# Kernel tuning notes

Hardware: AMD Instinct MI355X
Metric: run time of the kernel (lower is better)

## Reference

```python
import jax, jax.numpy as jnp
import numpy as np

EPS = 1e-8


def setup_inputs() -> dict:
    key = jax.random.key(0)
    ks = jax.random.split(key, 8)
    B, N, D = 8, 1024, 256
    x = jax.random.normal(ks[0], (B, N, D), dtype=jnp.float32)
    y = jax.random.normal(ks[1], (B, N, D), dtype=jnp.float32)
    coords = jax.random.normal(ks[2], (N, N, 6), dtype=jnp.float32)
    # xavier-ish init for U, kaiming-ish for S1/S2
    U = jax.random.normal(ks[3], (D, D), dtype=jnp.float32) * (1.0 / np.sqrt(D))
    S1 = jax.random.normal(ks[4], (D, 1), dtype=jnp.float32)
    S2 = jax.random.normal(ks[5], (D, 1), dtype=jnp.float32)
    gating = jnp.asarray(1.0, dtype=jnp.float32)
    h_temp = jnp.asarray(0.1, dtype=jnp.float32)
    p_temp = jnp.asarray(1.0, dtype=jnp.float32)
    # trunc_normal_(a=0, b=1): std-normal truncated to [0, 1]
    pos_emb = jax.random.truncated_normal(ks[6], 0.0, 1.0, (N, 6, 1)).astype(jnp.float32)
    return {"x": x, "y": y, "coords": coords, "U": U, "S1": S1, "S2": S2,
            "gating": gating, "h_temp": h_temp, "p_temp": p_temp, "pos_emb": pos_emb}


def _spectral(x, U, S):
    # x @ U.T @ diag(|S|) @ U  ==  ((x @ U.T) * |S|) @ U
    s = jnp.abs(S[:, 0])
    return ((x @ U.T) * s) @ U


def reference(x, y, coords, U, S1, S2, gating, h_temp, p_temp, pos_emb):
    B, N, D = x.shape
    scale = D ** (-0.5)
    xs = jnp.stack([_spectral(x, U, S1), _spectral(x, U, S2)], axis=1)  # [B,2,N,D]
    # patch attention scores: [B,2,N,N]
    patch_score = jax.nn.softmax(jnp.einsum('bknd,bmd->bknm', xs, y) * scale, axis=-1)
    # positional scores, shared across batch and the 2 spectral branches: [N,N]
    pos_logits = -jnp.abs(p_temp) * jnp.einsum('nmc,ncq->nm', coords, pos_emb)
    pos_score = jax.nn.softmax(pos_logits, axis=-1)
    g = jax.nn.sigmoid(gating)
    attn = (1.0 - g) * patch_score + g * pos_score[None, None]  # [B,2,N,N]
    # entropy over key axis -> [B,N,2]
    entropy = jnp.sum(-attn * jnp.log(attn + EPS), axis=-1).transpose(0, 2, 1)
    hmap = 2.0 - 2.0 * jax.nn.sigmoid(h_temp * entropy)  # [B,N,2]
    fgbg = hmap[..., 0] >= hmap[..., 1]
    route = jax.lax.stop_gradient(
        jnp.stack([fgbg, ~fgbg], axis=-1).astype(hmap.dtype))  # [B,N,2]
    heat_map = jnp.sum(hmap * route, axis=-1, keepdims=True)  # [B,N,1]
    attn_sel = jnp.sum(attn * route.transpose(0, 2, 1)[..., None], axis=1)  # [B,N,N]
    out = attn_sel @ y  # [B,N,D]
    return (out, heat_map)
```

## Files before the change

kernel.cpp:

```cpp
#include <hip/hip_runtime.h>
#include <hip/hip_bf16.h>
#include <stdint.h>


#define NB 8
#define NN_ 1024
#define ND 256

typedef __bf16 bf16x8 __attribute__((ext_vector_type(8)));
typedef __bf16 bf16x4 __attribute__((ext_vector_type(4)));
typedef float f32x4 __attribute__((ext_vector_type(4)));

__device__ inline void gl_lds(const __bf16* g, __bf16* l) {
    auto gp = (const __attribute__((address_space(1))) uint32_t*)(uintptr_t)g;
    auto lp = (__attribute__((address_space(3))) uint32_t*)(uintptr_t)l;
    __builtin_amdgcn_global_load_lds(gp, lp, 16, 0, 0);
}

__device__ inline float wred_sum(float v) {
#pragma unroll
    for (int o = 32; o; o >>= 1) v += __shfl_xor(v, o, 64);
    return v;
}
__device__ inline float wred_max(float v) {
#pragma unroll
    for (int o = 32; o; o >>= 1) v = fmaxf(v, __shfl_xor(v, o, 64));
    return v;
}

__global__ __launch_bounds__(256) void prep_kernel(
    const float* __restrict__ coords, const float* __restrict__ pos_emb,
    const float* __restrict__ p_temp, const float* __restrict__ x,
    const float* __restrict__ y, const float* __restrict__ U,
    const float* __restrict__ S1, const float* __restrict__ S2,
    float* __restrict__ posS, __bf16* __restrict__ Xh, __bf16* __restrict__ Xl,
    __bf16* __restrict__ yt, __bf16* __restrict__ Yh, __bf16* __restrict__ Yl,
    __bf16* __restrict__ Mh, __bf16* __restrict__ Ml) {
    __shared__ char sm[18432];
    const int bid = blockIdx.x;
    const int tid = threadIdx.x;

    if (bid < 256) {
        float* Us  = (float*)sm;
        float* s1s = Us + 16 * 256;
        float* s2s = s1s + 256;
        const int n = bid, j = tid;
        s1s[tid] = fabsf(S1[tid]);
        s2s[tid] = fabsf(S2[tid]);
        float a1 = 0.f, a2 = 0.f;
        for (int c0 = 0; c0 < ND; c0 += 16) {
            __syncthreads();
#pragma unroll
            for (int k = 0; k < 4; ++k) {
                const int idx = k * 256 + tid;
                ((float4*)Us)[idx] =
                    ((const float4*)(U + (long)c0 * ND))[idx];
            }
            __syncthreads();
#pragma unroll
            for (int cc = 0; cc < 16; ++cc) {
                const float un = Us[cc * 256 + n];
                const float uj = Us[cc * 256 + j];
                a1 = fmaf(s1s[c0 + cc] * un, uj, a1);
                a2 = fmaf(s2s[c0 + cc] * un, uj, a2);
            }
        }
        const __bf16 h1 = (__bf16)a1, h2 = (__bf16)a2;
        Mh[n * ND + j] = h1;           Ml[n * ND + j] = (__bf16)(a1 - (float)h1);
        Mh[65536 + n * ND + j] = h2;   Ml[65536 + n * ND + j] = (__bf16)(a2 - (float)h2);
    } else if (bid < 1280) {
        float* red = (float*)sm;
        const int n = bid - 256;
        const float pt = -fabsf(p_temp[0]);
        float pe[6];
#pragma unroll
        for (int c = 0; c < 6; ++c) pe[c] = pos_emb[n * 6 + c];
        const float* cr = coords + (long)n * NN_ * 6;
        float l[4];
#pragma unroll
        for (int j = 0; j < 4; ++j) {
            const int m = j * 256 + tid;
            const float2* cp = (const float2*)(cr + (long)m * 6);
            float2 c0 = cp[0], c1 = cp[1], c2 = cp[2];
            l[j] = pt * (c0.x * pe[0] + c0.y * pe[1] + c1.x * pe[2] +
                         c1.y * pe[3] + c2.x * pe[4] + c2.y * pe[5]);
        }
        float mx = fmaxf(fmaxf(l[0], l[1]), fmaxf(l[2], l[3]));
        mx = wred_max(mx);
        __syncthreads();
        if ((tid & 63) == 0) red[tid >> 6] = mx;
        __syncthreads();
        mx = fmaxf(fmaxf(red[0], red[1]), fmaxf(red[2], red[3]));
        float e[4], s = 0.f;
#pragma unroll
        for (int j = 0; j < 4; ++j) { e[j] = __expf(l[j] - mx); s += e[j]; }
        s = wred_sum(s);
        __syncthreads();
        if ((tid & 63) == 0) red[4 + (tid >> 6)] = s;
        __syncthreads();
        s = red[4] + red[5] + red[6] + red[7];
        const float inv = 1.f / s;
#pragma unroll
        for (int j = 0; j < 4; ++j)
            posS[(long)n * NN_ + j * 256 + tid] = e[j] * inv;
    } else if (bid < 1792) {
        const int n4 = NB * NN_ * ND / 4;
        int i = (bid - 1280) * 256 + tid;
        for (; i < n4; i += 512 * 256) {
            float4 v = ((const float4*)x)[i];
            bf16x4 h, l;
            h[0] = (__bf16)v.x; l[0] = (__bf16)(v.x - (float)h[0]);
            h[1] = (__bf16)v.y; l[1] = (__bf16)(v.y - (float)h[1]);
            h[2] = (__bf16)v.z; l[2] = (__bf16)(v.z - (float)h[2]);
            h[3] = (__bf16)v.w; l[3] = (__bf16)(v.w - (float)h[3]);
            ((bf16x4*)Xh)[i] = h;
            ((bf16x4*)Xl)[i] = l;
        }
    } else {
        __bf16 (*t)[72] = (__bf16(*)[72])sm;
        const int rem = bid - 1792;
        const int b = rem >> 6;
        const int m0 = (rem & 15) * 64, d0 = ((rem >> 4) & 3) * 64;
        const int c = tid & 15;
        const int r = tid >> 4;
#pragma unroll
        for (int p = 0; p < 4; ++p) {
            const int row = r + p * 16;
            const long gi = ((long)b * NN_ + m0 + row) * ND + d0 + c * 4;
            float4 v = *(const float4*)(y + gi);
            bf16x4 h, l;
            h[0] = (__bf16)v.x; l[0] = (__bf16)(v.x - (float)h[0]);
            h[1] = (__bf16)v.y; l[1] = (__bf16)(v.y - (float)h[1]);
            h[2] = (__bf16)v.z; l[2] = (__bf16)(v.z - (float)h[2]);
            h[3] = (__bf16)v.w; l[3] = (__bf16)(v.w - (float)h[3]);
            *(bf16x4*)(Yh + gi) = h;
            *(bf16x4*)(Yl + gi) = l;
            t[c * 4 + 0][row] = h[0]; t[c * 4 + 1][row] = h[1];
            t[c * 4 + 2][row] = h[2]; t[c * 4 + 3][row] = h[3];
        }
        __syncthreads();
#pragma unroll
        for (int p = 0; p < 4; ++p) {
            const int d = r + p * 16;
            bf16x4 o;
            o[0] = t[d][c * 4 + 0]; o[1] = t[d][c * 4 + 1];
            o[2] = t[d][c * 4 + 2]; o[3] = t[d][c * 4 + 3];
            *(bf16x4*)(yt + ((long)b * ND + d0 + d) * NN_ + m0 + c * 4) = o;
        }
    }
}

__global__ __launch_bounds__(256) void mgemm_xs(
    const __bf16* __restrict__ Ah, const __bf16* __restrict__ Al,
    const __bf16* __restrict__ Bh, const __bf16* __restrict__ Bl,
    __bf16* __restrict__ Ch, __bf16* __restrict__ Cl,
    int M, int N, int K, long sB1, long sC) {
    constexpr int BM = 64, BK = 32, BN = 64;
    __shared__ __bf16 As[2][2 * BM * BK];
    __shared__ __bf16 Bs[2][2 * BN * BK];

    const int z = blockIdx.z;
    Bh += (long)z * sB1; Bl += (long)z * sB1;

    const int tid = threadIdx.x;
    const int bm = blockIdx.y * BM, bn = blockIdx.x * BN;
    const int wave = tid >> 6, lane = tid & 63;
    const int wm = wave >> 1, wn = wave & 1;
    const int quad = lane >> 4, l16 = lane & 15;
    const int srow = lane >> 2, slot = lane & 3;

    f32x4 acc[2][2];
#pragma unroll
    for (int i = 0; i < 2; ++i)
#pragma unroll
        for (int j = 0; j < 2; ++j) acc[i][j] = (f32x4){0.f, 0.f, 0.f, 0.f};

    auto stage = [&](int sel, int k0) {
        const int r0 = wave * 16;
        const int row = r0 + srow;
        const int chunk = slot ^ ((row >> 1) & 3);
        const long ga = (long)(bm + row) * K + k0 + chunk * 8;
        gl_lds(Ah + ga, &As[sel][r0 * 32]);
        gl_lds(Al + ga, &As[sel][BM * BK + r0 * 32]);
        const long gb = (long)(bn + row) * K + k0 + chunk * 8;
        gl_lds(Bh + gb, &Bs[sel][r0 * 32]);
        gl_lds(Bl + gb, &Bs[sel][BN * BK + r0 * 32]);
    };

    stage(0, 0);
    __syncthreads();
    int cur = 0;
    for (int k0 = 0; k0 < K; k0 += BK) {
        if (k0 + BK < K) stage(cur ^ 1, k0 + BK);

        bf16x8 a_h[2], a_l[2], b_h[2], b_l[2];
#pragma unroll
        for (int mi = 0; mi < 2; ++mi) {
            const int row = wm * 32 + mi * 16 + l16;
            const int off = row * 32 + ((quad ^ ((row >> 1) & 3)) * 8);
            a_h[mi] = *(const bf16x8*)&As[cur][off];
            a_l[mi] = *(const bf16x8*)&As[cur][BM * BK + off];
        }
#pragma unroll
        for (int ni = 0; ni < 2; ++ni) {
            const int row = wn * 32 + ni * 16 + l16;
            const int off = row * 32 + ((quad ^ ((row >> 1) & 3)) * 8);
            b_h[ni] = *(const bf16x8*)&Bs[cur][off];
            b_l[ni] = *(const bf16x8*)&Bs[cur][BN * BK + off];
        }
#pragma unroll
        for (int mi = 0; mi < 2; ++mi)
#pragma unroll
            for (int ni = 0; ni < 2; ++ni) {
                acc[mi][ni] = __builtin_amdgcn_mfma_f32_16x16x32_bf16(
                    a_h[mi], b_h[ni], acc[mi][ni], 0, 0, 0);
                acc[mi][ni] = __builtin_amdgcn_mfma_f32_16x16x32_bf16(
                    a_h[mi], b_l[ni], acc[mi][ni], 0, 0, 0);
                acc[mi][ni] = __builtin_amdgcn_mfma_f32_16x16x32_bf16(
                    a_l[mi], b_h[ni], acc[mi][ni], 0, 0, 0);
            }

        __syncthreads();
        cur ^= 1;
    }

    Ch += (long)z * sC; Cl += (long)z * sC;
#pragma unroll
    for (int mi = 0; mi < 2; ++mi) {
        const int row0 = bm + wm * 32 + mi * 16 + quad * 4;
#pragma unroll
        for (int ni = 0; ni < 2; ++ni) {
            const int col = bn + wn * 32 + ni * 16 + l16;
#pragma unroll
            for (int r = 0; r < 4; ++r) {
                const float v = acc[mi][ni][r];
                const long idx = (long)(row0 + r) * N + col;
                const __bf16 h = (__bf16)v;
                Ch[idx] = h;
                Cl[idx] = (__bf16)(v - (float)h);
            }
        }
    }
}

__global__ __launch_bounds__(256) void mgemm_sc(
    const __bf16* __restrict__ Ah, const __bf16* __restrict__ Al,
    const __bf16* __restrict__ Bh, const __bf16* __restrict__ Bl,
    float* __restrict__ C, int N, int K,
    long sA1, long sA2, long sB1, long sC, float alpha) {
    constexpr int BM = 128, BK = 32, BN = 128;
    __shared__ __bf16 As[2 * BM * BK];
    __shared__ __bf16 Bs[2 * BN * BK];

    const int bid = blockIdx.x;
    const int xcd = bid & 7;
    const int j   = bid >> 3;
    const int z   = 2 * xcd + (j >> 6);
    const int t   = j & 63;
    const int bm  = (t >> 3) * BM;
    const int bn  = (t & 7) * BN;

    const long aoff = (long)(z >> 1) * sA1 + (long)(z & 1) * sA2;
    const long boff = (long)(z >> 1) * sB1;
    Ah += aoff; Al += aoff;
    Bh += boff; Bl += boff;

    const int tid = threadIdx.x;
    const int wave = tid >> 6, lane = tid & 63;
    const int wm = wave >> 1, wn = wave & 1;
    const int quad = lane >> 4, l16 = lane & 15;

    f32x4 acc[4][4];
#pragma unroll
    for (int i = 0; i < 4; ++i)
#pragma unroll
        for (int jj = 0; jj < 4; ++jj) acc[i][jj] = (f32x4){0.f, 0.f, 0.f, 0.f};

    const int srow = lane >> 2;
    const int slot = lane & 3;

    for (int k0 = 0; k0 < K; k0 += BK) {
        __syncthreads();
#pragma unroll
        for (int i = 0; i < 2; ++i) {
            const int r0 = wave * 32 + i * 16;
            const int row = r0 + srow;
            const int chunk = slot ^ ((row >> 1) & 3);
            const long ga = (long)(bm + row) * K + k0 + chunk * 8;
            gl_lds(Ah + ga, &As[r0 * 32]);
            gl_lds(Al + ga, &As[BM * BK + r0 * 32]);
            const long gb = (long)(bn + row) * K + k0 + chunk * 8;
            gl_lds(Bh + gb, &Bs[r0 * 32]);
            gl_lds(Bl + gb, &Bs[BN * BK + r0 * 32]);
        }
        __syncthreads();

        bf16x8 a_h[4], a_l[4], b_h[4], b_l[4];
#pragma unroll
        for (int mi = 0; mi < 4; ++mi) {
            const int row = wm * 64 + mi * 16 + l16;
            const int off = row * 32 + ((quad ^ ((row >> 1) & 3)) * 8);
            a_h[mi] = *(const bf16x8*)&As[off];
            a_l[mi] = *(const bf16x8*)&As[BM * BK + off];
        }
#pragma unroll
        for (int ni = 0; ni < 4; ++ni) {
            const int row = wn * 64 + ni * 16 + l16;
            const int off = row * 32 + ((quad ^ ((row >> 1) & 3)) * 8);
            b_h[ni] = *(const bf16x8*)&Bs[off];
            b_l[ni] = *(const bf16x8*)&Bs[BN * BK + off];
        }
#pragma unroll
        for (int mi = 0; mi < 4; ++mi)
#pragma unroll
            for (int ni = 0; ni < 4; ++ni) {
                acc[mi][ni] = __builtin_amdgcn_mfma_f32_16x16x32_bf16(
                    a_h[mi], b_h[ni], acc[mi][ni], 0, 0, 0);
                acc[mi][ni] = __builtin_amdgcn_mfma_f32_16x16x32_bf16(
                    a_h[mi], b_l[ni], acc[mi][ni], 0, 0, 0);
                acc[mi][ni] = __builtin_amdgcn_mfma_f32_16x16x32_bf16(
                    a_l[mi], b_h[ni], acc[mi][ni], 0, 0, 0);
            }
    }

    C += (long)z * sC;
#pragma unroll
    for (int mi = 0; mi < 4; ++mi) {
        const int row0 = bm + wm * 64 + mi * 16 + quad * 4;
#pragma unroll
        for (int ni = 0; ni < 4; ++ni) {
            const int col = bn + wn * 64 + ni * 16 + l16;
#pragma unroll
            for (int r = 0; r < 4; ++r)
                C[(long)(row0 + r) * NN_ + col] = acc[mi][ni][r] * alpha;
        }
    }
}

__global__ __launch_bounds__(256, 8) void blendsm_kernel(
    const float* __restrict__ S, const float* __restrict__ pos,
    const float* __restrict__ gating, const float* __restrict__ h_temp,
    __bf16* __restrict__ P, float* __restrict__ heat) {
    const int b = blockIdx.x & 7;
    const int n = (blockIdx.x >> 3) * 4 + (threadIdx.x >> 6);
    const int lane = threadIdx.x & 63;

    const float g = 1.f / (1.f + __expf(-gating[0]));
    const float cg = 1.f - g;
    const float ht = h_temp[0];

    const float* r0p = S + ((long)(b * 2 + 0) * NN_ + n) * NN_;
    const float* r1p = S + ((long)(b * 2 + 1) * NN_ + n) * NN_;

    f32x4 a0[4], a1[4];
#pragma unroll
    for (int j = 0; j < 4; ++j) {
        a0[j] = *(const f32x4*)(r0p + j * 256 + lane * 4);
        a1[j] = *(const f32x4*)(r1p + j * 256 + lane * 4);
    }
    float m0 = -3.4e38f, m1 = -3.4e38f;
#pragma unroll
    for (int j = 0; j < 4; ++j) {
        m0 = fmaxf(m0, fmaxf(fmaxf(a0[j][0], a0[j][1]), fmaxf(a0[j][2], a0[j][3])));
        m1 = fmaxf(m1, fmaxf(fmaxf(a1[j][0], a1[j][1]), fmaxf(a1[j][2], a1[j][3])));
    }
    m0 = wred_max(m0); m1 = wred_max(m1);
    float s0 = 0.f, s1 = 0.f;
#pragma unroll
    for (int j = 0; j < 4; ++j) {
        a0[j][0] = __expf(a0[j][0] - m0); a0[j][1] = __expf(a0[j][1] - m0);
        a0[j][2] = __expf(a0[j][2] - m0); a0[j][3] = __expf(a0[j][3] - m0);
        s0 += a0[j][0] + a0[j][1] + a0[j][2] + a0[j][3];
        a1[j][0] = __expf(a1[j][0] - m1); a1[j][1] = __expf(a1[j][1] - m1);
        a1[j][2] = __expf(a1[j][2] - m1); a1[j][3] = __expf(a1[j][3] - m1);
        s1 += a1[j][0] + a1[j][1] + a1[j][2] + a1[j][3];
    }
    s0 = wred_sum(s0); s1 = wred_sum(s1);
    const float i0 = 1.f / s0, i1 = 1.f / s1;
    const float* pr = pos + (long)n * NN_;
    float e0 = 0.f, e1 = 0.f;
#pragma unroll
    for (int j = 0; j < 4; ++j) {
        const f32x4 pv = *(const f32x4*)(pr + j * 256 + lane * 4);
        a0[j][0] = cg * a0[j][0] * i0 + g * pv[0];
        a0[j][1] = cg * a0[j][1] * i0 + g * pv[1];
        a0[j][2] = cg * a0[j][2] * i0 + g * pv[2];
        a0[j][3] = cg * a0[j][3] * i0 + g * pv[3];
        a1[j][0] = cg * a1[j][0] * i1 + g * pv[0];
        a1[j][1] = cg * a1[j][1] * i1 + g * pv[1];
        a1[j][2] = cg * a1[j][2] * i1 + g * pv[2];
        a1[j][3] = cg * a1[j][3] * i1 + g * pv[3];
        e0 -= a0[j][0] * __logf(a0[j][0] + 1e-8f) + a0[j][1] * __logf(a0[j][1] + 1e-8f) +
              a0[j][2] * __logf(a0[j][2] + 1e-8f) + a0[j][3] * __logf(a0[j][3] + 1e-8f);
        e1 -= a1[j][0] * __logf(a1[j][0] + 1e-8f) + a1[j][1] * __logf(a1[j][1] + 1e-8f) +
              a1[j][2] * __logf(a1[j][2] + 1e-8f) + a1[j][3] * __logf(a1[j][3] + 1e-8f);
    }
    e0 = wred_sum(e0); e1 = wred_sum(e1);
    const float hm0 = 2.f - 2.f / (1.f + __expf(-ht * e0));
    const float hm1 = 2.f - 2.f / (1.f + __expf(-ht * e1));
    const bool fg = (hm0 >= hm1);
    if (lane == 0) heat[(long)b * NN_ + n] = fg ? hm0 : hm1;
    __bf16* prow = P + ((long)b * NN_ + n) * NN_;
#pragma unroll
    for (int j = 0; j < 4; ++j) {
        const f32x4 v = fg ? a0[j] : a1[j];
        bf16x4 o;
        o[0] = (__bf16)v[0]; o[1] = (__bf16)v[1];
        o[2] = (__bf16)v[2]; o[3] = (__bf16)v[3];
        *(bf16x4*)(prow + j * 256 + lane * 4) = o;
    }
}

__global__ __launch_bounds__(256) void pv_gemm(
    const __bf16* __restrict__ A, const __bf16* __restrict__ Bm,
    float* __restrict__ C) {
    constexpr int BM = 32, BK = 32, BN = 64;
    __shared__ __bf16 As[2][BM * BK];
    __shared__ __bf16 Bs[2][BN * BK];

    const int bid = blockIdx.x;
    const int b   = bid & 7;
    const int j   = bid >> 3;
    const int bm  = (j >> 2) * BM;
    const int bn  = (j & 3) * BN;

    A  += (long)b * NN_ * NN_;
    Bm += (long)b * ND * NN_;
    C  += (long)b * NN_ * ND;

    const int tid = threadIdx.x;
    const int wave = tid >> 6, lane = tid & 63;
    const int wm = wave >> 1, wn = wave & 1;
    const int quad = lane >> 4, l16 = lane & 15;
    const int srow = lane >> 2, slot = lane & 3;

    f32x4 acc[2];
    acc[0] = (f32x4){0.f, 0.f, 0.f, 0.f};
    acc[1] = (f32x4){0.f, 0.f, 0.f, 0.f};

    auto stage = [&](int sel, int k0) {
        if (wave < 2) {
            const int row = wave * 16 + srow;
            const int chunk = slot ^ ((row >> 1) & 3);
            gl_lds(A + (long)(bm + row) * NN_ + k0 + chunk * 8,
                   &As[sel][wave * 16 * 32]);
        }
        {
            const int row = wave * 16 + srow;
            const int chunk = slot ^ ((row >> 1) & 3);
            gl_lds(Bm + (long)(bn + row) * NN_ + k0 + chunk * 8,
                   &Bs[sel][wave * 16 * 32]);
        }
    };

    stage(0, 0);
    __syncthreads();
    int cur = 0;
    for (int k0 = 0; k0 < NN_; k0 += BK) {
        if (k0 + BK < NN_) stage(cur ^ 1, k0 + BK);

        const int arow = wm * 16 + l16;
        const int aoff = arow * 32 + ((quad ^ ((arow >> 1) & 3)) * 8);
        bf16x8 a = *(const bf16x8*)&As[cur][aoff];
#pragma unroll
        for (int ni = 0; ni < 2; ++ni) {
            const int brow = wn * 32 + ni * 16 + l16;
            const int boff = brow * 32 + ((quad ^ ((brow >> 1) & 3)) * 8);
            bf16x8 bb = *(const bf16x8*)&Bs[cur][boff];
            acc[ni] = __builtin_amdgcn_mfma_f32_16x16x32_bf16(
                a, bb, acc[ni], 0, 0, 0);
        }

        __syncthreads();
        cur ^= 1;
    }

    const int row0 = bm + wm * 16 + quad * 4;
#pragma unroll
    for (int ni = 0; ni < 2; ++ni) {
        const int col = bn + wn * 32 + ni * 16 + l16;
#pragma unroll
        for (int r = 0; r < 4; ++r)
            C[(long)(row0 + r) * ND + col] = acc[ni][r];
    }
}

extern "C" void kernel_launch(void* const* d_in, const int* in_sizes, int n_in,
                              void* d_out, int out_size, void* d_ws, size_t ws_size,
                              hipStream_t stream) {
    const float* x      = (const float*)d_in[0];
    const float* y      = (const float*)d_in[1];
    const float* coords = (const float*)d_in[2];
    const float* U      = (const float*)d_in[3];
    const float* S1p    = (const float*)d_in[4];
    const float* S2p    = (const float*)d_in[5];
    const float* gating = (const float*)d_in[6];
    const float* h_temp = (const float*)d_in[7];
    const float* p_temp = (const float*)d_in[8];
    const float* pos_emb= (const float*)d_in[9];

    float* out  = (float*)d_out;
    float* heat = out + (long)NB * NN_ * ND;

    char* ws = (char*)d_ws;
    const long MB = 1 << 20;
    float*  Sf  = (float*)(ws);
    float*  pos = (float*)(ws + 64 * MB);
    __bf16* Xh  = (__bf16*)(ws + 68 * MB);
    __bf16* Xl  = (__bf16*)(ws + 72 * MB);
    __bf16* XSh = (__bf16*)(ws + 76 * MB);
    __bf16* XSl = (__bf16*)(ws + 84 * MB);
    __bf16* yt  = (__bf16*)(ws + 92 * MB);
    __bf16* Yh  = (__bf16*)(ws + 96 * MB);
    __bf16* Yl  = (__bf16*)(ws + 100 * MB);
    __bf16* Mh  = (__bf16*)(ws + 104 * MB);
    __bf16* Ml  = Mh + 2 * 65536;
    __bf16* Pb  = (__bf16*)(ws + 76 * MB);

    const long ND2 = (long)NN_ * ND;
    const long BND = (long)NB * ND2;

    prep_kernel<<<dim3(2304), 256, 0, stream>>>(
        coords, pos_emb, p_temp, x, y, U, S1p, S2p,
        pos, Xh, Xl, yt, Yh, Yl, Mh, Ml);

    mgemm_xs<<<dim3(4, 128, 2), 256, 0, stream>>>(
        Xh, Xl, Mh, Ml, XSh, XSl, NB * NN_, ND, ND, 65536, BND);

    mgemm_sc<<<dim3(1024), 256, 0, stream>>>(
        XSh, XSl, Yh, Yl, Sf, NN_, ND,
        ND2, BND, ND2, (long)NN_ * NN_, 0.0625f);

    blendsm_kernel<<<dim3(2048), 256, 0, stream>>>(
        Sf, pos, gating, h_temp, Pb, heat);

    pv_gemm<<<dim3(1024), 256, 0, stream>>>(Pb, yt, out);

    (void)in_sizes; (void)n_in; (void)out_size; (void)ws_size;
}
```

Baseline: 188.7 us.

## Double-buffer LDS in score GEMM and halve N tile to double grid

The score GEMM kernel now stages the next K-slice into a second LDS buffer while computing on the current one, using a single barrier per iteration instead of two. The N tile shrinks from 128 to 64, so each block holds half the accumulators and the launch doubles to 2048 blocks, with the block-to-tile mapping adjusted to match. The aim is to hide global-to-LDS latency and raise occupancy and wave count. In exchange, B-operand reuse per block drops and total A-tile traffic doubles.

```diff
diff --git a/kernel.cpp b/kernel.cpp
--- a/kernel.cpp
+++ b/kernel.cpp
@@ -248,17 +248,17 @@
     const __bf16* __restrict__ Bh, const __bf16* __restrict__ Bl,
     float* __restrict__ C, int N, int K,
     long sA1, long sA2, long sB1, long sC, float alpha) {
-    constexpr int BM = 128, BK = 32, BN = 128;
-    __shared__ __bf16 As[2 * BM * BK];
-    __shared__ __bf16 Bs[2 * BN * BK];
+    constexpr int BM = 128, BK = 32, BN = 64;
+    __shared__ __bf16 As[2][2 * BM * BK];
+    __shared__ __bf16 Bs[2][2 * BN * BK];
 
     const int bid = blockIdx.x;
     const int xcd = bid & 7;
     const int j   = bid >> 3;
-    const int z   = 2 * xcd + (j >> 6);
-    const int t   = j & 63;
-    const int bm  = (t >> 3) * BM;
-    const int bn  = (t & 7) * BN;
+    const int z   = 2 * xcd + (j >> 7);
+    const int t   = j & 127;
+    const int bm  = (t >> 4) * BM;
+    const int bn  = (t & 15) * BN;
 
     const long aoff = (long)(z >> 1) * sA1 + (long)(z & 1) * sA2;
     const long boff = (long)(z >> 1) * sB1;
@@ -269,51 +269,59 @@
     const int wave = tid >> 6, lane = tid & 63;
     const int wm = wave >> 1, wn = wave & 1;
     const int quad = lane >> 4, l16 = lane & 15;
-
-    f32x4 acc[4][4];
+    const int srow = lane >> 2, slot = lane & 3;
+
+    f32x4 acc[4][2];
 #pragma unroll
     for (int i = 0; i < 4; ++i)
 #pragma unroll
-        for (int jj = 0; jj < 4; ++jj) acc[i][jj] = (f32x4){0.f, 0.f, 0.f, 0.f};
-
-    const int srow = lane >> 2;
-    const int slot = lane & 3;
-
-    for (int k0 = 0; k0 < K; k0 += BK) {
-        __syncthreads();
+        for (int jj = 0; jj < 2; ++jj) acc[i][jj] = (f32x4){0.f, 0.f, 0.f, 0.f};
+
+    auto stage = [&](int sel, int k0) {
 #pragma unroll
         for (int i = 0; i < 2; ++i) {
             const int r0 = wave * 32 + i * 16;
             const int row = r0 + srow;
             const int chunk = slot ^ ((row >> 1) & 3);
             const long ga = (long)(bm + row) * K + k0 + chunk * 8;
-            gl_lds(Ah + ga, &As[r0 * 32]);
-            gl_lds(Al + ga, &As[BM * BK + r0 * 32]);
+            gl_lds(Ah + ga, &As[sel][r0 * 32]);
+            gl_lds(Al + ga, &As[sel][BM * BK + r0 * 32]);
+        }
+        {
+            const int r0 = wave * 16;
+            const int row = r0 + srow;
+            const int chunk = slot ^ ((row >> 1) & 3);
             const long gb = (long)(bn + row) * K + k0 + chunk * 8;
-            gl_lds(Bh + gb, &Bs[r0 * 32]);
-            gl_lds(Bl + gb, &Bs[BN * BK + r0 * 32]);
-        }
-        __syncthreads();
-
-        bf16x8 a_h[4], a_l[4], b_h[4], b_l[4];
+            gl_lds(Bh + gb, &Bs[sel][r0 * 32]);
+            gl_lds(Bl + gb, &Bs[sel][BN * BK + r0 * 32]);
+        }
+    };
+
+    stage(0, 0);
+    __syncthreads();
+    int cur = 0;
+    for (int k0 = 0; k0 < K; k0 += BK) {
+        if (k0 + BK < K) stage(cur ^ 1, k0 + BK);
+
+        bf16x8 a_h[4], a_l[4], b_h[2], b_l[2];
 #pragma unroll
         for (int mi = 0; mi < 4; ++mi) {
             const int row = wm * 64 + mi * 16 + l16;
             const int off = row * 32 + ((quad ^ ((row >> 1) & 3)) * 8);
-            a_h[mi] = *(const bf16x8*)&As[off];
-            a_l[mi] = *(const bf16x8*)&As[BM * BK + off];
-        }
-#pragma unroll
-        for (int ni = 0; ni < 4; ++ni) {
-            const int row = wn * 64 + ni * 16 + l16;
+            a_h[mi] = *(const bf16x8*)&As[cur][off];
+            a_l[mi] = *(const bf16x8*)&As[cur][BM * BK + off];
+        }
+#pragma unroll
+        for (int ni = 0; ni < 2; ++ni) {
+            const int row = wn * 32 + ni * 16 + l16;
             const int off = row * 32 + ((quad ^ ((row >> 1) & 3)) * 8);
-            b_h[ni] = *(const bf16x8*)&Bs[off];
-            b_l[ni] = *(const bf16x8*)&Bs[BN * BK + off];
+            b_h[ni] = *(const bf16x8*)&Bs[cur][off];
+            b_l[ni] = *(const bf16x8*)&Bs[cur][BN * BK + off];
         }
 #pragma unroll
         for (int mi = 0; mi < 4; ++mi)
 #pragma unroll
-            for (int ni = 0; ni < 4; ++ni) {
+            for (int ni = 0; ni < 2; ++ni) {
                 acc[mi][ni] = __builtin_amdgcn_mfma_f32_16x16x32_bf16(
                     a_h[mi], b_h[ni], acc[mi][ni], 0, 0, 0);
                 acc[mi][ni] = __builtin_amdgcn_mfma_f32_16x16x32_bf16(
@@ -321,6 +329,9 @@
                 acc[mi][ni] = __builtin_amdgcn_mfma_f32_16x16x32_bf16(
                     a_l[mi], b_h[ni], acc[mi][ni], 0, 0, 0);
             }
+
+        __syncthreads();
+        cur ^= 1;
     }
 
     C += (long)z * sC;
@@ -328,8 +339,8 @@
     for (int mi = 0; mi < 4; ++mi) {
         const int row0 = bm + wm * 64 + mi * 16 + quad * 4;
 #pragma unroll
-        for (int ni = 0; ni < 4; ++ni) {
-            const int col = bn + wn * 64 + ni * 16 + l16;
+        for (int ni = 0; ni < 2; ++ni) {
+            const int col = bn + wn * 32 + ni * 16 + l16;
 #pragma unroll
             for (int r = 0; r < 4; ++r)
                 C[(long)(row0 + r) * NN_ + col] = acc[mi][ni][r] * alpha;
@@ -527,7 +538,7 @@
     mgemm_xs<<<dim3(4, 128, 2), 256, 0, stream>>>(
         Xh, Xl, Mh, Ml, XSh, XSl, NB * NN_, ND, ND, 65536, BND);
 
-    mgemm_sc<<<dim3(1024), 256, 0, stream>>>(
+    mgemm_sc<<<dim3(2048), 256, 0, stream>>>(
         XSh, XSl, Yh, Yl, Sf, NN_, ND,
         ND2, BND, ND2, (long)NN_ * NN_, 0.0625f);
 
```

New measurement: 191.7 us. No clear change (+1.6%).
